# Optimization experiments

Hardware: AMD Instinct MI355X
Metric: run time of the kernel (lower is better)

## Reference

```python
import jax, jax.numpy as jnp
import numpy as np

N_EMBD = 1024
HEAD_SIZE = 64
B, T = 8, 2048


def setup_inputs() -> dict:
    key = jax.random.key(0)
    k1, k2, k3, k4 = jax.random.split(key, 4)
    scale = 1.0 / np.sqrt(N_EMBD)
    return {
        "x": jax.random.normal(k1, (B, T, N_EMBD), dtype=jnp.float32),
        "Wq": jax.random.normal(k2, (N_EMBD, HEAD_SIZE), dtype=jnp.float32) * scale,
        "Wk": jax.random.normal(k3, (N_EMBD, HEAD_SIZE), dtype=jnp.float32) * scale,
        "Wv": jax.random.normal(k4, (N_EMBD, HEAD_SIZE), dtype=jnp.float32) * scale,
    }


def reference(x, Wq, Wk, Wv):
    # x: [B, T, C]; projections (no bias)
    q = jnp.einsum("btc,ch->bth", x, Wq)
    k = jnp.einsum("btc,ch->bth", x, Wk)
    v = jnp.einsum("btc,ch->bth", x, Wv)
    head_size = k.shape[-1]
    # scaled scores [B, T, T]
    wei = jnp.einsum("bth,bsh->bts", q, k) * (head_size ** -0.5)
    # causal mask (lower-triangular keeps)
    Tlen = x.shape[1]
    causal = jnp.tril(jnp.ones((Tlen, Tlen), dtype=bool))
    wei = jnp.where(causal[None, :, :], wei, -jnp.inf)
    wei = jax.nn.softmax(wei, axis=-1)
    # dropout p=0 (eval) -> identity
    out = jnp.einsum("bts,bsh->bth", wei, v)
    return out
```

## Files before the change

kernel.cpp:

```cpp
#include <hip/hip_runtime.h>
#include <hip/hip_bf16.h>
#include <math.h>

#define Bn 8
#define Tn 2048
#define Cn 1024
#define Hn 64

typedef __attribute__((ext_vector_type(8))) short short8;
typedef __attribute__((ext_vector_type(4))) float floatx4;
typedef __attribute__((ext_vector_type(8))) _Float16 half8;

#define ATTN_SCALE 0.18033688011112042f

__device__ inline unsigned short f2bf(float f) {
    union { float f; unsigned int u; } x; x.f = f;
    unsigned int r = x.u + 0x7fffu + ((x.u >> 16) & 1u);
    return (unsigned short)(r >> 16);
}

__device__ inline uint2 pack4bf(float4 v) {
    __hip_bfloat162 lo = __float22bfloat162_rn(make_float2(v.x, v.y));
    __hip_bfloat162 hi = __float22bfloat162_rn(make_float2(v.z, v.w));
    uint2 r;
    r.x = *reinterpret_cast<unsigned int*>(&lo);
    r.y = *reinterpret_cast<unsigned int*>(&hi);
    return r;
}

__global__ __launch_bounds__(256) void prep_w(
    const float* __restrict__ Wq, const float* __restrict__ Wk,
    const float* __restrict__ Wv, unsigned short* __restrict__ Wfrag)
{
    const int gid = blockIdx.x * 256 + threadIdx.x;
    const int c    = gid >> 11;
    const int rem  = gid & 2047;
    const int ks   = rem >> 6;
    const int lane = rem & 63;
    const int ln = lane & 15, qd = lane >> 4;
    const int mat = c >> 2, nc = c & 3;
    const float* W = (mat == 0) ? Wq : (mat == 1) ? Wk : Wv;
    const float sc = (mat == 0) ? ATTN_SCALE : 1.0f;
    const int col = nc * 16 + ln;
    unsigned short o[8];
    #pragma unroll
    for (int j = 0; j < 8; ++j)
        o[j] = f2bf(W[(size_t)(ks * 32 + qd * 8 + j) * Hn + col] * sc);
    *reinterpret_cast<short8*>(Wfrag + (size_t)gid * 8) = *reinterpret_cast<short8*>(o);
}

__global__ __launch_bounds__(256, 4) void proj_mfma(
    const float* __restrict__ x, const unsigned short* __restrict__ Wfrag,
    unsigned short* __restrict__ qbf, unsigned short* __restrict__ kfrag,
    unsigned short* __restrict__ vfrag)
{
    __shared__ unsigned short xs[32 * 512];

    const int ln   = threadIdx.x & 15;
    const int quad = (threadIdx.x >> 4) & 3;
    const int w    = threadIdx.x >> 6;
    const int lane = threadIdx.x & 63;
    const int row0 = blockIdx.x * 16;

    const int srow = threadIdx.x >> 4;
    const int sf   = threadIdx.x & 15;
    const float4* xrow4 = reinterpret_cast<const float4*>(x + (size_t)(row0 + srow) * Cn);

    float4 ld[16];
    #pragma unroll
    for (int it = 0; it < 16; ++it)
        ld[it] = xrow4[sf + 16 * it];
    #pragma unroll
    for (int it = 0; it < 16; ++it) {
        const int f4g = sf + 16 * it;
        const int s = f4g >> 3;
        const int q = (f4g >> 1) & 3;
        const int j = (f4g & 1) * 4;
        *reinterpret_cast<uint2*>(&xs[s * 512 + (q * 16 + srow) * 8 + j]) = pack4bf(ld[it]);
    }
    __syncthreads();

    floatx4 acc[3];
    #pragma unroll
    for (int i = 0; i < 3; ++i) acc[i] = (floatx4){0.f, 0.f, 0.f, 0.f};

    #pragma unroll 4
    for (int s = 0; s < 32; ++s) {
        const short8 a = *reinterpret_cast<const short8*>(&xs[s * 512 + lane * 8]);
        #pragma unroll
        for (int i = 0; i < 3; ++i) {
            const int cc = w * 3 + i;
            const short8 b = *reinterpret_cast<const short8*>(
                Wfrag + ((size_t)(cc * 32 + s) * 64 + lane) * 8);
            acc[i] = __builtin_amdgcn_mfma_f32_16x16x32_bf16(a, b, acc[i], 0, 0, 0);
        }
    }

    const int t0   = row0 + quad * 4;
    const int b    = t0 >> 11;
    const int tloc = t0 & 2047;
    #pragma unroll
    for (int i = 0; i < 3; ++i) {
        const int idx = w * 3 + i;
        const int mat = idx >> 2, ch = idx & 3;
        if (mat == 0) {
            #pragma unroll
            for (int r = 0; r < 4; ++r)
                qbf[(size_t)(t0 + r) * Hn + ch * 16 + ln] = f2bf(acc[i][r]);
        } else if (mat == 1) {
            const int kc = tloc >> 4;
            const int ks = ch >> 1;
            const int lq = (ch & 1) * 2 + (ln >> 3);
            #pragma unroll
            for (int r = 0; r < 4; ++r) {
                const int lanep = (quad * 4 + r) + 16 * lq;
                kfrag[(((size_t)(b * 128 + kc) * 2 + ks) * 64 + lanep) * 8 + (ln & 7)]
                    = f2bf(acc[i][r]);
            }
        } else {
            const int t32 = tloc >> 5;
            const int h16 = (tloc >> 4) & 1;
            union { _Float16 h[4]; ushort4 u; } cv;
            cv.h[0] = (_Float16)acc[i][0]; cv.h[1] = (_Float16)acc[i][1];
            cv.h[2] = (_Float16)acc[i][2]; cv.h[3] = (_Float16)acc[i][3];
            *reinterpret_cast<ushort4*>(
                vfrag + (((size_t)(b * 64 + t32) * 4 + ch) * 64 + ln + 16 * quad) * 8
                      + h16 * 4) = cv.u;
        }
    }
}

__global__ __launch_bounds__(256, 4) void attn_mfma(
    const unsigned short* __restrict__ qbf, const unsigned short* __restrict__ kfrag,
    const unsigned short* __restrict__ vfrag, float* __restrict__ out)
{
    __shared__ float o_lds[4][16][68];
    __shared__ float l_lds[4][16];

    const int j  = blockIdx.x;
    const int b  = j & 7;
    const int ti = 127 - (j >> 3);
    const int q0 = ti * 16;

    const int ln   = threadIdx.x & 15;
    const int quad = (threadIdx.x >> 4) & 3;
    const int w    = threadIdx.x >> 6;
    const int lane = threadIdx.x & 63;

    const unsigned short* qb = qbf + (size_t)b * Tn * Hn;
    const unsigned short* Kb = kfrag + (size_t)b * 131072;
    const unsigned short* Vb = vfrag + (size_t)b * 131072;

    const short8 aq0 = *reinterpret_cast<const short8*>(qb + (size_t)(q0 + ln) * Hn + quad * 8);
    const short8 aq1 = *reinterpret_cast<const short8*>(qb + (size_t)(q0 + ln) * Hn + 32 + quad * 8);

    floatx4 O[4];
    #pragma unroll
    for (int c = 0; c < 4; ++c) O[c] = (floatx4){0.f, 0.f, 0.f, 0.f};
    float lp = 0.f;

    const int ntiles = (q0 + 47) >> 5;
    const int per    = (ntiles + 3) >> 2;
    const int beg    = w * per;
    const int end    = min(beg + per, ntiles);

    short8 kf[4]; half8 vf[4];
    if (beg < end) {
        #pragma unroll
        for (int u = 0; u < 4; ++u) {
            kf[u] = *reinterpret_cast<const short8*>(Kb + (size_t)(beg * 4 + u) * 512 + lane * 8);
            vf[u] = *reinterpret_cast<const half8*>(Vb + (size_t)(beg * 4 + u) * 512 + lane * 8);
        }
    }

    for (int t = beg; t < end; ++t) {
        const int tn = (t + 1 < end) ? (t + 1) : t;
        short8 kn[4]; half8 vn[4];
        #pragma unroll
        for (int u = 0; u < 4; ++u) {
            kn[u] = *reinterpret_cast<const short8*>(Kb + (size_t)(tn * 4 + u) * 512 + lane * 8);
            vn[u] = *reinterpret_cast<const half8*>(Vb + (size_t)(tn * 4 + u) * 512 + lane * 8);
        }

        const floatx4 z = (floatx4){0.f, 0.f, 0.f, 0.f};
        floatx4 St0 = __builtin_amdgcn_mfma_f32_16x16x32_bf16(kf[0], aq0, z, 0, 0, 0);
        St0 = __builtin_amdgcn_mfma_f32_16x16x32_bf16(kf[1], aq1, St0, 0, 0, 0);
        floatx4 St1 = __builtin_amdgcn_mfma_f32_16x16x32_bf16(kf[2], aq0, z, 0, 0, 0);
        St1 = __builtin_amdgcn_mfma_f32_16x16x32_bf16(kf[3], aq1, St1, 0, 0, 0);

        const bool diag = (t == ntiles - 1);
        const int koff = t * 32 - q0;
        half8 pa;
        #pragma unroll
        for (int r = 0; r < 4; ++r) {
            float s0 = St0[r], s1 = St1[r];
            if (diag) {
                if (koff + quad * 4 + r > ln)      s0 = -1e30f;
                if (koff + 16 + quad * 4 + r > ln) s1 = -1e30f;
            }
            const float p0 = exp2f(s0);
            const float p1 = exp2f(s1);
            lp += p0 + p1;
            pa[r]     = (_Float16)p0;
            pa[r + 4] = (_Float16)p1;
        }
        #pragma unroll
        for (int c = 0; c < 4; ++c)
            O[c] = __builtin_amdgcn_mfma_f32_16x16x32_f16(pa, vf[c], O[c], 0, 0, 0);

        #pragma unroll
        for (int u = 0; u < 4; ++u) { kf[u] = kn[u]; vf[u] = vn[u]; }
    }

    #pragma unroll
    for (int c = 0; c < 4; ++c)
        #pragma unroll
        for (int r = 0; r < 4; ++r)
            o_lds[w][quad * 4 + r][c * 16 + ln] = O[c][r];
    {
        float lt = lp;
        lt += __shfl_xor(lt, 16);
        lt += __shfl_xor(lt, 32);
        if (quad == 0) l_lds[w][ln] = lt;
    }
    __syncthreads();

    const int qq = threadIdx.x >> 4;
    const int dg = threadIdx.x & 15;
    const float ltot = l_lds[0][qq] + l_lds[1][qq] + l_lds[2][qq] + l_lds[3][qq];
    const float inv = 1.0f / ltot;
    const float4 a0 = *reinterpret_cast<float4*>(&o_lds[0][qq][dg * 4]);
    const float4 a1 = *reinterpret_cast<float4*>(&o_lds[1][qq][dg * 4]);
    const float4 a2 = *reinterpret_cast<float4*>(&o_lds[2][qq][dg * 4]);
    const float4 a3 = *reinterpret_cast<float4*>(&o_lds[3][qq][dg * 4]);
    float4 r;
    r.x = (a0.x + a1.x + a2.x + a3.x) * inv;
    r.y = (a0.y + a1.y + a2.y + a3.y) * inv;
    r.z = (a0.z + a1.z + a2.z + a3.z) * inv;
    r.w = (a0.w + a1.w + a2.w + a3.w) * inv;
    *reinterpret_cast<float4*>(out + ((size_t)b * Tn + q0 + qq) * Hn + dg * 4) = r;
}

extern "C" void kernel_launch(void* const* d_in, const int* in_sizes, int n_in,
                              void* d_out, int out_size, void* d_ws, size_t ws_size,
                              hipStream_t stream) {
    (void)in_sizes; (void)n_in; (void)out_size; (void)ws_size;
    const float* x  = (const float*)d_in[0];
    const float* Wq = (const float*)d_in[1];
    const float* Wk = (const float*)d_in[2];
    const float* Wv = (const float*)d_in[3];
    float* out = (float*)d_out;

    unsigned short* Wfrag = (unsigned short*)d_ws;
    unsigned short* qbf   = Wfrag + (size_t)196608;
    unsigned short* kfr   = qbf + (size_t)Bn * Tn * Hn;
    unsigned short* vfr   = kfr + (size_t)Bn * 131072;

    prep_w<<<96, 256, 0, stream>>>(Wq, Wk, Wv, Wfrag);
    proj_mfma<<<(Bn * Tn) / 16, 256, 0, stream>>>(x, Wfrag, qbf, kfr, vfr);
    attn_mfma<<<Bn * (Tn / 16), 256, 0, stream>>>(qbf, kfr, vfr, out);
}
```

Baseline: 125.6 us.

## Process 32 query rows per attention block to reuse K/V fragments

Each attention block now handles two 16-row query tiles instead of one, so every K/V fragment loaded from global memory feeds twice as many MFMAs. The grid is halved and the causal mask on the diagonal tile is rewritten for the 32-row tile. The epilogue reduction is extended to 32 rows with wider per-thread writes. In exchange, register use goes up (launch bounds drop to 2 blocks per SM), and fewer, longer blocks may balance the causal triangle less evenly.

```diff
diff --git a/kernel.cpp b/kernel.cpp
--- a/kernel.cpp
+++ b/kernel.cpp
@@ -130,17 +130,17 @@
     }
 }
 
-__global__ __launch_bounds__(256, 4) void attn_mfma(
+__global__ __launch_bounds__(256, 2) void attn_mfma(
     const unsigned short* __restrict__ qbf, const unsigned short* __restrict__ kfrag,
     const unsigned short* __restrict__ vfrag, float* __restrict__ out)
 {
-    __shared__ float o_lds[4][16][68];
-    __shared__ float l_lds[4][16];
+    __shared__ float o_lds[4][32][68];
+    __shared__ float l_lds[4][32];
 
     const int j  = blockIdx.x;
     const int b  = j & 7;
-    const int ti = 127 - (j >> 3);
-    const int q0 = ti * 16;
+    const int qg = 63 - (j >> 3);
+    const int q0 = qg * 32;
 
     const int ln   = threadIdx.x & 15;
     const int quad = (threadIdx.x >> 4) & 3;
@@ -151,15 +151,22 @@
     const unsigned short* Kb = kfrag + (size_t)b * 131072;
     const unsigned short* Vb = vfrag + (size_t)b * 131072;
 
-    const short8 aq0 = *reinterpret_cast<const short8*>(qb + (size_t)(q0 + ln) * Hn + quad * 8);
-    const short8 aq1 = *reinterpret_cast<const short8*>(qb + (size_t)(q0 + ln) * Hn + 32 + quad * 8);
-
-    floatx4 O[4];
-    #pragma unroll
-    for (int c = 0; c < 4; ++c) O[c] = (floatx4){0.f, 0.f, 0.f, 0.f};
-    float lp = 0.f;
-
-    const int ntiles = (q0 + 47) >> 5;
+    short8 aq[2][2];
+    #pragma unroll
+    for (int m = 0; m < 2; ++m)
+        #pragma unroll
+        for (int h = 0; h < 2; ++h)
+            aq[m][h] = *reinterpret_cast<const short8*>(
+                qb + (size_t)(q0 + m * 16 + ln) * Hn + h * 32 + quad * 8);
+
+    floatx4 O[2][4];
+    #pragma unroll
+    for (int m = 0; m < 2; ++m)
+        #pragma unroll
+        for (int c = 0; c < 4; ++c) O[m][c] = (floatx4){0.f, 0.f, 0.f, 0.f};
+    float lp[2] = {0.f, 0.f};
+
+    const int ntiles = qg + 1;
     const int per    = (ntiles + 3) >> 2;
     const int beg    = w * per;
     const int end    = min(beg + per, ntiles);
@@ -182,63 +189,70 @@
             vn[u] = *reinterpret_cast<const half8*>(Vb + (size_t)(tn * 4 + u) * 512 + lane * 8);
         }
 
+        const bool diag = (t == ntiles - 1);
         const floatx4 z = (floatx4){0.f, 0.f, 0.f, 0.f};
-        floatx4 St0 = __builtin_amdgcn_mfma_f32_16x16x32_bf16(kf[0], aq0, z, 0, 0, 0);
-        St0 = __builtin_amdgcn_mfma_f32_16x16x32_bf16(kf[1], aq1, St0, 0, 0, 0);
-        floatx4 St1 = __builtin_amdgcn_mfma_f32_16x16x32_bf16(kf[2], aq0, z, 0, 0, 0);
-        St1 = __builtin_amdgcn_mfma_f32_16x16x32_bf16(kf[3], aq1, St1, 0, 0, 0);
-
-        const bool diag = (t == ntiles - 1);
-        const int koff = t * 32 - q0;
-        half8 pa;
-        #pragma unroll
-        for (int r = 0; r < 4; ++r) {
-            float s0 = St0[r], s1 = St1[r];
-            if (diag) {
-                if (koff + quad * 4 + r > ln)      s0 = -1e30f;
-                if (koff + 16 + quad * 4 + r > ln) s1 = -1e30f;
+        #pragma unroll
+        for (int m = 0; m < 2; ++m) {
+            floatx4 St0 = __builtin_amdgcn_mfma_f32_16x16x32_bf16(kf[0], aq[m][0], z, 0, 0, 0);
+            St0 = __builtin_amdgcn_mfma_f32_16x16x32_bf16(kf[1], aq[m][1], St0, 0, 0, 0);
+            floatx4 St1 = __builtin_amdgcn_mfma_f32_16x16x32_bf16(kf[2], aq[m][0], z, 0, 0, 0);
+            St1 = __builtin_amdgcn_mfma_f32_16x16x32_bf16(kf[3], aq[m][1], St1, 0, 0, 0);
+
+            half8 pa;
+            #pragma unroll
+            for (int r = 0; r < 4; ++r) {
+                float s0 = St0[r], s1 = St1[r];
+                if (diag) {
+                    if (quad * 4 + r > m * 16 + ln)      s0 = -1e30f;
+                    if (16 + quad * 4 + r > m * 16 + ln) s1 = -1e30f;
+                }
+                const float p0 = exp2f(s0);
+                const float p1 = exp2f(s1);
+                lp[m] += p0 + p1;
+                pa[r]     = (_Float16)p0;
+                pa[r + 4] = (_Float16)p1;
             }
-            const float p0 = exp2f(s0);
-            const float p1 = exp2f(s1);
-            lp += p0 + p1;
-            pa[r]     = (_Float16)p0;
-            pa[r + 4] = (_Float16)p1;
-        }
+            #pragma unroll
+            for (int c = 0; c < 4; ++c)
+                O[m][c] = __builtin_amdgcn_mfma_f32_16x16x32_f16(pa, vf[c], O[m][c], 0, 0, 0);
+        }
+
+        #pragma unroll
+        for (int u = 0; u < 4; ++u) { kf[u] = kn[u]; vf[u] = vn[u]; }
+    }
+
+    #pragma unroll
+    for (int m = 0; m < 2; ++m) {
         #pragma unroll
         for (int c = 0; c < 4; ++c)
-            O[c] = __builtin_amdgcn_mfma_f32_16x16x32_f16(pa, vf[c], O[c], 0, 0, 0);
-
-        #pragma unroll
-        for (int u = 0; u < 4; ++u) { kf[u] = kn[u]; vf[u] = vn[u]; }
-    }
-
-    #pragma unroll
-    for (int c = 0; c < 4; ++c)
-        #pragma unroll
-        for (int r = 0; r < 4; ++r)
-            o_lds[w][quad * 4 + r][c * 16 + ln] = O[c][r];
-    {
-        float lt = lp;
+            #pragma unroll
+            for (int r = 0; r < 4; ++r)
+                o_lds[w][m * 16 + quad * 4 + r][c * 16 + ln] = O[m][c][r];
+        float lt = lp[m];
         lt += __shfl_xor(lt, 16);
         lt += __shfl_xor(lt, 32);
-        if (quad == 0) l_lds[w][ln] = lt;
+        if (quad == 0) l_lds[w][m * 16 + ln] = lt;
     }
     __syncthreads();
 
-    const int qq = threadIdx.x >> 4;
-    const int dg = threadIdx.x & 15;
+    const int qq  = threadIdx.x >> 3;
+    const int dgp = threadIdx.x & 7;
     const float ltot = l_lds[0][qq] + l_lds[1][qq] + l_lds[2][qq] + l_lds[3][qq];
     const float inv = 1.0f / ltot;
-    const float4 a0 = *reinterpret_cast<float4*>(&o_lds[0][qq][dg * 4]);
-    const float4 a1 = *reinterpret_cast<float4*>(&o_lds[1][qq][dg * 4]);
-    const float4 a2 = *reinterpret_cast<float4*>(&o_lds[2][qq][dg * 4]);
-    const float4 a3 = *reinterpret_cast<float4*>(&o_lds[3][qq][dg * 4]);
-    float4 r;
-    r.x = (a0.x + a1.x + a2.x + a3.x) * inv;
-    r.y = (a0.y + a1.y + a2.y + a3.y) * inv;
-    r.z = (a0.z + a1.z + a2.z + a3.z) * inv;
-    r.w = (a0.w + a1.w + a2.w + a3.w) * inv;
-    *reinterpret_cast<float4*>(out + ((size_t)b * Tn + q0 + qq) * Hn + dg * 4) = r;
+    float* op = out + ((size_t)b * Tn + q0 + qq) * Hn + dgp * 8;
+    #pragma unroll
+    for (int u = 0; u < 2; ++u) {
+        const float4 a0 = *reinterpret_cast<float4*>(&o_lds[0][qq][dgp * 8 + u * 4]);
+        const float4 a1 = *reinterpret_cast<float4*>(&o_lds[1][qq][dgp * 8 + u * 4]);
+        const float4 a2 = *reinterpret_cast<float4*>(&o_lds[2][qq][dgp * 8 + u * 4]);
+        const float4 a3 = *reinterpret_cast<float4*>(&o_lds[3][qq][dgp * 8 + u * 4]);
+        float4 r;
+        r.x = (a0.x + a1.x + a2.x + a3.x) * inv;
+        r.y = (a0.y + a1.y + a2.y + a3.y) * inv;
+        r.z = (a0.z + a1.z + a2.z + a3.z) * inv;
+        r.w = (a0.w + a1.w + a2.w + a3.w) * inv;
+        *reinterpret_cast<float4*>(op + u * 4) = r;
+    }
 }
 
 extern "C" void kernel_launch(void* const* d_in, const int* in_sizes, int n_in,
@@ -258,5 +272,5 @@
 
     prep_w<<<96, 256, 0, stream>>>(Wq, Wk, Wv, Wfrag);
     proj_mfma<<<(Bn * Tn) / 16, 256, 0, stream>>>(x, Wfrag, qbf, kfr, vfr);
-    attn_mfma<<<Bn * (Tn / 16), 256, 0, stream>>>(qbf, kfr, vfr, out);
-}
+    attn_mfma<<<Bn * (Tn / 32), 256, 0, stream>>>(qbf, kfr, vfr, out);
+}
```

Result: no change. 127.2 us (+1.2%).
